# Kernel optimization log

Measured on AMD Instinct MI355X. Metric: run time of the kernel, lower is better.

The kernel has to match this reference:

```python
import jax, jax.numpy as jnp
import numpy as np

N, DIM, K = 131072, 64, 1024


def setup_inputs() -> dict:
    key = jax.random.key(0)
    kx, ke = jax.random.split(key)
    x = jax.random.normal(kx, (N, DIM), dtype=jnp.float32)
    # codebook buffer, initialized like uniform(-1/K, 1/K) in the original
    scale = 1.0 / K
    embedding = jax.random.uniform(ke, (K, DIM), dtype=jnp.float32, minval=-scale, maxval=scale)
    return {"x": x, "embedding": embedding}


def reference(x, embedding):
    # squared euclidean distances in fp32 (matches compute_distances)
    x32 = x.astype(jnp.float32)
    e32 = embedding.astype(jnp.float32)
    distances = (
        jnp.sum(x32 * x32, axis=1, keepdims=True)
        + jnp.sum(e32 * e32, axis=1)
        - 2.0 * jnp.einsum("nd,kd->nk", x32, e32)
    )
    indices = jnp.argmin(distances, axis=1)          # (N,)
    quantized = embedding[indices]                    # (N, DIM) codebook gather
    # commitment loss: mse(stop_grad(quantized), x)
    commitment_loss = jnp.mean((jax.lax.stop_gradient(quantized) - x) ** 2)
    # straight-through estimator
    quantized_st = x + jax.lax.stop_gradient(quantized - x)
    return quantized_st, indices, commitment_loss
```

## Files before the change

kernel.cpp:

```cpp
#include <hip/hip_runtime.h>
#include <hip/hip_bf16.h>

#define N_ROWS 131072
#define DIM 64
#define K_CODES 1024
#define NTILES 64
#define MARGIN 4e-5f
#define LIST_CAP 65536

typedef short short8 __attribute__((ext_vector_type(8)));
typedef float f32x4 __attribute__((ext_vector_type(4)));
typedef const __attribute__((address_space(1))) void* gptr_t;
typedef __attribute__((address_space(3))) void* lptr_t;

__device__ __forceinline__ unsigned short f2bf(float f) {
    unsigned u = __float_as_uint(f);
    return (unsigned short)((u + 0x7fffu + ((u >> 16) & 1u)) >> 16);
}
__device__ __forceinline__ float bf2f(unsigned short h) {
    return __uint_as_float(((unsigned)h) << 16);
}

__device__ __forceinline__ float np_sq64(const float* __restrict__ v) {
    float xx[DIM];
    #pragma unroll
    for (int d = 0; d < DIM; ++d) xx[d] = v[d] * v[d];
    float r[8];
    #pragma unroll
    for (int j = 0; j < 8; ++j) r[j] = xx[j];
    #pragma unroll
    for (int i = 8; i < DIM; i += 8)
        #pragma unroll
        for (int j = 0; j < 8; ++j) r[j] = r[j] + xx[i + j];
    return ((r[0]+r[1]) + (r[2]+r[3])) + ((r[4]+r[5]) + (r[6]+r[7]));
}

__device__ __forceinline__ float np_dot64(const float* __restrict__ xv,
                                          const float* __restrict__ ek) {
    float a0 = 0.f, a1 = 0.f, a2 = 0.f, a3 = 0.f;
    #pragma unroll
    for (int c = 0; c < DIM; c += 16)
        #pragma unroll
        for (int b = 12; b >= 0; b -= 4) {
            const int d = c + b;
            a0 = a0 + xv[d+0] * ek[d+0];
            a1 = a1 + xv[d+1] * ek[d+1];
            a2 = a2 + xv[d+2] * ek[d+2];
            a3 = a3 + xv[d+3] * ek[d+3];
        }
    return (a0 + a1) + (a2 + a3);
}


__global__ void vq_prep(const float* __restrict__ emb, float* __restrict__ esq,
                        unsigned short* __restrict__ wsB,
                        unsigned int* __restrict__ cnt, float* __restrict__ loss) {
#pragma clang fp contract(off)
    const int t = blockIdx.x * blockDim.x + threadIdx.x;
    if (t == 0) { *cnt = 0u; *loss = 0.f; }
    const int k = t >> 2, c = t & 3;
    if (k >= K_CODES) return;
    const float* e = emb + (size_t)k * DIM;

    if (c == 0) esq[k] = np_sq64(e);

    const int off = (c & 1) * 32, sel = c >> 1;
    unsigned short val[32];
    #pragma unroll
    for (int j = 0; j < 32; ++j) {
        float v = e[off + j];
        unsigned short h = f2bf(v);
        val[j] = sel ? f2bf(v - bf2f(h)) : h;
    }
    const int tile = k >> 4, n = k & 15;
    #pragma unroll
    for (int g = 0; g < 4; ++g) {
        short8 s;
        #pragma unroll
        for (int j = 0; j < 8; ++j) s[j] = (short)val[g*8 + j];
        *reinterpret_cast<short8*>(wsB + ((size_t)((tile*4 + c)*64 + g*16 + n)) * 8) = s;
    }
}

__global__ __launch_bounds__(256, 2) void vq_mfma(const float* __restrict__ x,
        const float* __restrict__ emb, const float* __restrict__ esq,
        const unsigned short* __restrict__ wsB, float* __restrict__ out,
        unsigned int* __restrict__ cnt, unsigned int* __restrict__ list,
        float* __restrict__ loss) {
#pragma clang fp contract(off)
    const int tid = threadIdx.x;
    const int lane = tid & 63;
    const int w = tid >> 6;
    const int g = lane >> 4, res = lane & 15;
    const int rowbase = blockIdx.x * 256 + w * 64;

    __shared__ __align__(16) unsigned char sB[4][4][4096];
    __shared__ float s_esq[K_CODES];
    __shared__ float s_k1[256], s_k2[256], s_k3[256], s_k4[256];
    __shared__ int s_idx[256];

    for (int i = tid; i < K_CODES; i += 256) s_esq[i] = esq[i];
    __syncthreads();

    short8 Ah[4][2], Al[4][2];
    #pragma unroll
    for (int rg = 0; rg < 4; ++rg) {
        const float* xr = x + (size_t)(rowbase + rg*16 + res) * DIM;
        #pragma unroll
        for (int h = 0; h < 2; ++h) {
            float4 v0 = *reinterpret_cast<const float4*>(xr + h*32 + g*8);
            float4 v1 = *reinterpret_cast<const float4*>(xr + h*32 + g*8 + 4);
            float xv[8] = {v0.x, v0.y, v0.z, v0.w, v1.x, v1.y, v1.z, v1.w};
            short8 sh, sl;
            #pragma unroll
            for (int j = 0; j < 8; ++j) {
                unsigned short hb = f2bf(xv[j]);
                sh[j] = (short)hb;
                sl[j] = (short)f2bf(xv[j] - bf2f(hb));
            }
            Ah[rg][h] = sh; Al[rg][h] = sl;
        }
    }

    const unsigned char* wsBb = (const unsigned char*)wsB;
    auto stage = [&](int ct, int slot) {
        const unsigned char* src = wsBb + (size_t)ct * 4096 + lane * 16;
        #pragma unroll
        for (int c = 0; c < 4; ++c)
            __builtin_amdgcn_global_load_lds((gptr_t)(src + c * 1024),
                                             (lptr_t)&sB[w][slot][c * 1024], 16, 0, 0);
    };
    auto readB = [&](short8* Bd, int slot) {
        #pragma unroll
        for (int c = 0; c < 4; ++c)
            Bd[c] = *reinterpret_cast<const short8*>(&sB[w][slot][c * 1024 + lane * 16]);
    };

    float b1[16], b2[16], b3[16], b4[16];
    const float FINF = __uint_as_float(0x7F800000u);
    #pragma unroll
    for (int s = 0; s < 16; ++s) { b1[s]=FINF; b2[s]=FINF; b3[s]=FINF; b4[s]=FINF; }

    auto MF = [&](f32x4* acc, const short8* B) {
        __builtin_amdgcn_s_setprio(1);
        #pragma unroll
        for (int rg = 0; rg < 4; ++rg) acc[rg] = f32x4{0.f, 0.f, 0.f, 0.f};
        #pragma unroll
        for (int rg = 0; rg < 4; ++rg)
            acc[rg] = __builtin_amdgcn_mfma_f32_16x16x32_bf16(Ah[rg][0], B[0], acc[rg], 0,0,0);
        #pragma unroll
        for (int rg = 0; rg < 4; ++rg)
            acc[rg] = __builtin_amdgcn_mfma_f32_16x16x32_bf16(Ah[rg][1], B[1], acc[rg], 0,0,0);
        #pragma unroll
        for (int rg = 0; rg < 4; ++rg)
            acc[rg] = __builtin_amdgcn_mfma_f32_16x16x32_bf16(Ah[rg][0], B[2], acc[rg], 0,0,0);
        #pragma unroll
        for (int rg = 0; rg < 4; ++rg)
            acc[rg] = __builtin_amdgcn_mfma_f32_16x16x32_bf16(Ah[rg][1], B[3], acc[rg], 0,0,0);
        #pragma unroll
        for (int rg = 0; rg < 4; ++rg)
            acc[rg] = __builtin_amdgcn_mfma_f32_16x16x32_bf16(Al[rg][0], B[0], acc[rg], 0,0,0);
        #pragma unroll
        for (int rg = 0; rg < 4; ++rg)
            acc[rg] = __builtin_amdgcn_mfma_f32_16x16x32_bf16(Al[rg][1], B[1], acc[rg], 0,0,0);
        __builtin_amdgcn_s_setprio(0);
    };

    auto KY = [&](const f32x4* acc, float esqv, int ct) {
        const unsigned kcur = (unsigned)(ct*16 + res);
        #pragma unroll
        for (int rg = 0; rg < 4; ++rg) {
            #pragma unroll
            for (int r = 0; r < 4; ++r) {
                float v = fmaf(-2.0f, acc[rg][r], esqv);
                float key = __uint_as_float((__float_as_uint(v) & 0xFFFFFC00u) | kcur);
                const int s = rg*4 + r;
                float o1 = b1[s], o2 = b2[s], o3 = b3[s];
                b4[s] = __builtin_amdgcn_fmed3f(key, o3, b4[s]);
                b3[s] = __builtin_amdgcn_fmed3f(key, o2, o3);
                b2[s] = __builtin_amdgcn_fmed3f(key, o1, o2);
                b1[s] = fminf(o1, key);
            }
        }
    };

    stage(0, 0); stage(1, 1); stage(2, 2);
    float e0 = s_esq[res], e1 = s_esq[16 + res];

    short8 Bc[4];
    f32x4 accA[4], accB[4];

    stage(3, 3);
    asm volatile("s_waitcnt vmcnt(12)" ::: "memory");
    readB(Bc, 0);
    MF(accA, Bc);

    for (int p = 0; p < 30; ++p) {
        const int t = 2 * p + 1;
        stage(t + 3, (t + 3) & 3);
        asm volatile("s_waitcnt vmcnt(12)" ::: "memory");
        readB(Bc, t & 3);
        MF(accB, Bc);
        KY(accA, e0, t - 1);  e0 = s_esq[(t + 1) * 16 + res];
        stage(t + 4, (t + 4) & 3);
        asm volatile("s_waitcnt vmcnt(12)" ::: "memory");
        readB(Bc, (t + 1) & 3);
        MF(accA, Bc);
        KY(accB, e1, t);      e1 = s_esq[(t + 2) * 16 + res];
    }
    asm volatile("s_waitcnt vmcnt(8)" ::: "memory");
    readB(Bc, 1);
    MF(accB, Bc);
    KY(accA, e0, 60);  e0 = s_esq[62 * 16 + res];
    asm volatile("s_waitcnt vmcnt(4)" ::: "memory");
    readB(Bc, 2);
    MF(accA, Bc);
    KY(accB, e1, 61);  e1 = s_esq[63 * 16 + res];
    asm volatile("s_waitcnt vmcnt(0)" ::: "memory");
    readB(Bc, 3);
    MF(accB, Bc);
    KY(accA, e0, 62);
    KY(accB, e1, 63);

    #pragma unroll
    for (int m = 1; m < 16; m <<= 1) {
        #pragma unroll
        for (int s = 0; s < 16; ++s) {
            float oa1 = __shfl_xor(b1[s], m, 64);
            float oa2 = __shfl_xor(b2[s], m, 64);
            float oa3 = __shfl_xor(b3[s], m, 64);
            float oa4 = __shfl_xor(b4[s], m, 64);
            float m1 = fminf(b1[s], oa1);
            float m2 = fminf(fmaxf(b1[s], oa1), fminf(b2[s], oa2));
            float m3 = fminf(fminf(fmaxf(b1[s], oa2), fmaxf(b2[s], oa1)),
                             fminf(b3[s], oa3));
            float m4 = fminf(fminf(fmaxf(b1[s], oa3), fmaxf(b3[s], oa1)),
                             fminf(fmaxf(b2[s], oa2), fminf(b4[s], oa4)));
            b1[s] = m1; b2[s] = m2; b3[s] = m3; b4[s] = m4;
        }
    }

    if (res == 0) {
        #pragma unroll
        for (int s = 0; s < 16; ++s) {
            const int rl = w*64 + (s >> 2)*16 + g*4 + (s & 3);
            s_k1[rl] = b1[s]; s_k2[rl] = b2[s]; s_k3[rl] = b3[s]; s_k4[rl] = b4[s];
        }
    }
    __syncthreads();

    {
        const int row = blockIdx.x * 256 + tid;
        unsigned u1 = __float_as_uint(s_k1[tid]);
        unsigned u2 = __float_as_uint(s_k2[tid]);
        unsigned u3 = __float_as_uint(s_k3[tid]);
        unsigned u4 = __float_as_uint(s_k4[tid]);
        float f1 = __uint_as_float(u1 & 0xFFFFFC00u);
        float f2 = __uint_as_float(u2 & 0xFFFFFC00u);
        float f3 = __uint_as_float(u3 & 0xFFFFFC00u);
        float f4 = __uint_as_float(u4 & 0xFFFFFC00u);
        int idx;
        if (f4 - f1 < MARGIN) {
            unsigned slot = atomicAdd(cnt, 1u);
            if (slot < LIST_CAP) list[slot] = (unsigned)row;
            idx = -1;
        } else if (f2 - f1 < MARGIN) {
            const int nc = (f3 - f1 < MARGIN) ? 3 : 2;
            int cand[3] = {(int)(u1 & 0x3FFu), (int)(u2 & 0x3FFu), (int)(u3 & 0x3FFu)};
            float xv[DIM];
            const float4* xp = reinterpret_cast<const float4*>(x + (size_t)row * DIM);
            #pragma unroll
            for (int q = 0; q < 16; ++q) {
                float4 v = xp[q];
                xv[4*q+0] = v.x; xv[4*q+1] = v.y; xv[4*q+2] = v.z; xv[4*q+3] = v.w;
            }
            float xsq = np_sq64(xv);
            float bd = INFINITY; int bi = 0x7fffffff;
            for (int c = 0; c < nc; ++c) {
                const int k = cand[c];
                float tt = xsq + s_esq[k];
                float dd = tt - 2.0f * np_dot64(xv, emb + (size_t)k * DIM);
                if (dd < bd || (dd == bd && k < bi)) { bd = dd; bi = k; }
            }
            idx = bi;
        } else {
            idx = (int)(u1 & 0x3FFu);
        }
        s_idx[tid] = idx;
    }
    __syncthreads();

    float lsum = 0.f;
    #pragma unroll
    for (int pass = 0; pass < 2; ++pass) {
        const int rl = (tid >> 1) + pass * 128, half = tid & 1;
        const int row = blockIdx.x * 256 + rl;
        const int idx = s_idx[rl];
        if (idx >= 0) {
            const float* xr = x + (size_t)row * DIM + half*32;
            const float* qr = emb + (size_t)idx * DIM + half*32;
            float* orow = out + (size_t)row * DIM + half*32;
            #pragma unroll
            for (int i = 0; i < 8; ++i) {
                float4 xv = reinterpret_cast<const float4*>(xr)[i];
                float4 qv = reinterpret_cast<const float4*>(qr)[i];
                float df0 = qv.x - xv.x, df1 = qv.y - xv.y;
                float df2 = qv.z - xv.z, df3 = qv.w - xv.w;
                lsum = fmaf(df0, df0, lsum); lsum = fmaf(df1, df1, lsum);
                lsum = fmaf(df2, df2, lsum); lsum = fmaf(df3, df3, lsum);
                float4 o = {xv.x + df0, xv.y + df1, xv.z + df2, xv.w + df3};
                reinterpret_cast<float4*>(orow)[i] = o;
            }
            if (half == 0) out[(size_t)N_ROWS * DIM + row] = (float)idx;
        }
    }
    #pragma unroll
    for (int off = 32; off > 0; off >>= 1) lsum += __shfl_down(lsum, off, 64);
    if (lane == 0) atomicAdd(loss, lsum);
}

__global__ void vq_fixup(const float* __restrict__ x, const float* __restrict__ emb,
                         const float* __restrict__ esq,
                         const unsigned int* __restrict__ cnt,
                         const unsigned int* __restrict__ list,
                         float* __restrict__ out, float* __restrict__ loss) {
#pragma clang fp contract(off)
    const int lane = threadIdx.x & 63;
    const int wid = (blockIdx.x * blockDim.x + threadIdx.x) >> 6;
    const int nw = (256 * 256) >> 6;
    unsigned count = *cnt;
    if (count > LIST_CAP) count = LIST_CAP;
    for (unsigned i = wid; i < count; i += nw) {
        const int row = (int)list[i];
        float xv[DIM];
        const float4* xp = reinterpret_cast<const float4*>(x + (size_t)row * DIM);
        #pragma unroll
        for (int q = 0; q < 16; ++q) {
            float4 v = xp[q];
            xv[4*q+0] = v.x; xv[4*q+1] = v.y; xv[4*q+2] = v.z; xv[4*q+3] = v.w;
        }
        float xsq = np_sq64(xv);
        float best = INFINITY; int bidx = 0x7fffffff;
        for (int t = 0; t < K_CODES / 64; ++t) {
            const int k = lane + t * 64;
            float dot = np_dot64(xv, emb + (size_t)k * DIM);
            float tt = xsq + esq[k];
            float dist = tt - 2.0f * dot;
            if (dist < best) { best = dist; bidx = k; }
        }
        #pragma unroll
        for (int m = 1; m < 64; m <<= 1) {
            float ob = __shfl_xor(best, m, 64);
            int   oi = __shfl_xor(bidx, m, 64);
            if (ob < best || (ob == best && oi < bidx)) { best = ob; bidx = oi; }
        }
        const float xd = x[(size_t)row * DIM + lane];
        const float qd = emb[(size_t)bidx * DIM + lane];
        const float df = qd - xd;
        out[(size_t)row * DIM + lane] = xd + df;
        if (lane == 0) out[(size_t)N_ROWS * DIM + row] = (float)bidx;
        float l2 = df * df;
        #pragma unroll
        for (int off = 32; off > 0; off >>= 1) l2 += __shfl_down(l2, off, 64);
        if (lane == 0) atomicAdd(loss, l2);
    }
}

__global__ void vq_final(const float* __restrict__ loss_acc, float* __restrict__ out_loss) {
    if (threadIdx.x == 0 && blockIdx.x == 0)
        out_loss[0] = loss_acc[0] / (float)((size_t)N_ROWS * DIM);
}

extern "C" void kernel_launch(void* const* d_in, const int* in_sizes, int n_in,
                              void* d_out, int out_size, void* d_ws, size_t ws_size,
                              hipStream_t stream) {
    const float* x   = (const float*)d_in[0];
    const float* emb = (const float*)d_in[1];
    float* out = (float*)d_out;

    unsigned int* cnt  = (unsigned int*)d_ws;
    float* loss        = (float*)d_ws + 1;
    float* esq         = (float*)d_ws + 4;
    unsigned short* wsB = (unsigned short*)((char*)d_ws + 8192);
    unsigned int* list = (unsigned int*)((char*)d_ws + 270336);

    vq_prep<<<dim3(64), dim3(64), 0, stream>>>(emb, esq, wsB, cnt, loss);
    vq_mfma<<<dim3(N_ROWS / 256), dim3(256), 0, stream>>>(x, emb, esq, wsB, out,
                                                          cnt, list, loss);
    vq_fixup<<<dim3(256), dim3(256), 0, stream>>>(x, emb, esq, cnt, list, out, loss);
    vq_final<<<dim3(1), dim3(1), 0, stream>>>(loss, out + (size_t)N_ROWS * DIM + N_ROWS);
}
```

Baseline: 145.1 us.

## Share codebook tile staging across waves with a 5-slot barrier-synced LDS ring

Previously each of the four waves staged its own copy of every codebook tile into LDS. Now all 256 threads load each 4 KB tile cooperatively into one shared 5-slot ring, with a vmcnt wait and block barrier per tile. This cuts global/L2 traffic for the codebook by the number of waves and shrinks LDS use, at the cost of a block-wide barrier per tile. The per-code norms are read straight from global memory instead of an LDS copy, and the top-4 update for the previous tile is issued before the next MFMA batch.

```diff
diff --git a/kernel.cpp b/kernel.cpp
--- a/kernel.cpp
+++ b/kernel.cpp
@@ -81,6 +81,9 @@
         *reinterpret_cast<short8*>(wsB + ((size_t)((tile*4 + c)*64 + g*16 + n)) * 8) = s;
     }
 }
+
+#define VM(N) asm volatile("s_waitcnt vmcnt(" #N ")" ::: "memory")
+#define BAR() __builtin_amdgcn_s_barrier()
 
 __global__ __launch_bounds__(256, 2) void vq_mfma(const float* __restrict__ x,
         const float* __restrict__ emb, const float* __restrict__ esq,
@@ -94,13 +97,9 @@
     const int g = lane >> 4, res = lane & 15;
     const int rowbase = blockIdx.x * 256 + w * 64;
 
-    __shared__ __align__(16) unsigned char sB[4][4][4096];
-    __shared__ float s_esq[K_CODES];
+    __shared__ __align__(16) unsigned char sB[5][4096];
     __shared__ float s_k1[256], s_k2[256], s_k3[256], s_k4[256];
     __shared__ int s_idx[256];
-
-    for (int i = tid; i < K_CODES; i += 256) s_esq[i] = esq[i];
-    __syncthreads();
 
     short8 Ah[4][2], Al[4][2];
     #pragma unroll
@@ -124,16 +123,13 @@
 
     const unsigned char* wsBb = (const unsigned char*)wsB;
     auto stage = [&](int ct, int slot) {
-        const unsigned char* src = wsBb + (size_t)ct * 4096 + lane * 16;
-        #pragma unroll
-        for (int c = 0; c < 4; ++c)
-            __builtin_amdgcn_global_load_lds((gptr_t)(src + c * 1024),
-                                             (lptr_t)&sB[w][slot][c * 1024], 16, 0, 0);
+        __builtin_amdgcn_global_load_lds((gptr_t)(wsBb + (size_t)ct * 4096 + tid * 16),
+                                         (lptr_t)&sB[slot][tid * 16], 16, 0, 0);
     };
     auto readB = [&](short8* Bd, int slot) {
         #pragma unroll
         for (int c = 0; c < 4; ++c)
-            Bd[c] = *reinterpret_cast<const short8*>(&sB[w][slot][c * 1024 + lane * 16]);
+            Bd[c] = *reinterpret_cast<const short8*>(&sB[slot][c * 1024 + lane * 16]);
     };
 
     float b1[16], b2[16], b3[16], b4[16];
@@ -184,42 +180,44 @@
         }
     };
 
-    stage(0, 0); stage(1, 1); stage(2, 2);
-    float e0 = s_esq[res], e1 = s_esq[16 + res];
-
     short8 Bc[4];
     f32x4 accA[4], accB[4];
-
-    stage(3, 3);
-    asm volatile("s_waitcnt vmcnt(12)" ::: "memory");
+    float e0 = esq[res], e1 = esq[16 + res];
+
+    stage(0, 0); stage(1, 1); stage(2, 2);
+
+    stage(3, 3); VM(3); BAR();
     readB(Bc, 0);
     MF(accA, Bc);
 
+    int slr = 1;
     for (int p = 0; p < 30; ++p) {
-        const int t = 2 * p + 1;
-        stage(t + 3, (t + 3) & 3);
-        asm volatile("s_waitcnt vmcnt(12)" ::: "memory");
-        readB(Bc, t & 3);
+        const int t0 = 2*p + 1;
+        int ss0 = slr + 3; if (ss0 >= 5) ss0 -= 5;
+        int ss1 = slr + 4; if (ss1 >= 5) ss1 -= 5;
+        int slr1 = slr + 1; if (slr1 >= 5) slr1 -= 5;
+        stage(t0 + 3, ss0); VM(3); BAR();
+        readB(Bc, slr);
+        KY(accA, e0, t0 - 1);  e0 = esq[(t0 + 1) * 16 + res];
         MF(accB, Bc);
-        KY(accA, e0, t - 1);  e0 = s_esq[(t + 1) * 16 + res];
-        stage(t + 4, (t + 4) & 3);
-        asm volatile("s_waitcnt vmcnt(12)" ::: "memory");
-        readB(Bc, (t + 1) & 3);
+        stage(t0 + 4, ss1); VM(3); BAR();
+        readB(Bc, slr1);
+        KY(accB, e1, t0);      e1 = esq[(t0 + 2) * 16 + res];
         MF(accA, Bc);
-        KY(accB, e1, t);      e1 = s_esq[(t + 2) * 16 + res];
-    }
-    asm volatile("s_waitcnt vmcnt(8)" ::: "memory");
+        slr += 2; if (slr >= 5) slr -= 5;
+    }
+    VM(2); BAR();
     readB(Bc, 1);
+    KY(accA, e0, 60);  e0 = esq[62 * 16 + res];
     MF(accB, Bc);
-    KY(accA, e0, 60);  e0 = s_esq[62 * 16 + res];
-    asm volatile("s_waitcnt vmcnt(4)" ::: "memory");
+    VM(1); BAR();
     readB(Bc, 2);
+    KY(accB, e1, 61);  e1 = esq[63 * 16 + res];
     MF(accA, Bc);
-    KY(accB, e1, 61);  e1 = s_esq[63 * 16 + res];
-    asm volatile("s_waitcnt vmcnt(0)" ::: "memory");
+    VM(0); BAR();
     readB(Bc, 3);
+    KY(accA, e0, 62);
     MF(accB, Bc);
-    KY(accA, e0, 62);
     KY(accB, e1, 63);
 
     #pragma unroll
@@ -278,7 +276,7 @@
             float bd = INFINITY; int bi = 0x7fffffff;
             for (int c = 0; c < nc; ++c) {
                 const int k = cand[c];
-                float tt = xsq + s_esq[k];
+                float tt = xsq + esq[k];
                 float dd = tt - 2.0f * np_dot64(xv, emb + (size_t)k * DIM);
                 if (dd < bd || (dd == bd && k < bi)) { bd = dd; bi = k; }
             }
```

Measured after the change: 135.2 us. -6.9%, faster.
